# Kernel optimization log

Hardware: AMD Instinct MI355X
Metric: run time of the kernel (lower is better)

Reference implementation:

```python
import jax, jax.numpy as jnp
import numpy as np

FEATURE_DIM = 256
LN_EPS = 1e-5        # torch nn.LayerNorm default
WHITEN_EPS = 1e-4    # whitening_eps init arg


def setup_inputs() -> dict:
    key = jax.random.key(0)
    k1, _ = jax.random.split(key)
    B, T, D = 64, 2048, FEATURE_DIM
    x = jax.random.normal(k1, (B, T, D), dtype=jnp.float32)
    gamma = jnp.ones((D,), dtype=jnp.float32)
    beta = jnp.zeros((D,), dtype=jnp.float32)
    return {"x": x, "gamma": gamma, "beta": beta}


def reference(x, gamma, beta):
    # x: (B, T, D)
    B, T, D = x.shape
    # LayerNorm over last dim
    mean = jnp.mean(x, axis=-1, keepdims=True)
    var = jnp.mean((x - mean) ** 2, axis=-1, keepdims=True)
    xn = (x - mean) * jax.lax.rsqrt(var + LN_EPS) * gamma + beta
    # Batched cross-frame covariance whitening (T >= 2 here)
    mu = jnp.mean(xn, axis=1, keepdims=True)          # (B, 1, D)
    xc = xn - mu                                       # (B, T, D)
    cov = jnp.einsum('btd,bte->bde', xc, xc) / (T - 1) # (B, D, D)
    cov = cov + WHITEN_EPS * jnp.eye(D, dtype=x.dtype)
    eigvals, eigvecs = jnp.linalg.eigh(cov)            # (B, D), (B, D, D)
    inv_sqrt_vals = jax.lax.rsqrt(jnp.clip(eigvals, WHITEN_EPS, None))  # (B, D)
    # inv_sqrt = V diag(w^-1/2) V^T
    inv_sqrt = jnp.einsum('bde,be,bfe->bdf', eigvecs, inv_sqrt_vals, eigvecs)
    out = jnp.einsum('btd,bdf->btf', xc, inv_sqrt)
    return out
```

## Files before the change

kernel.cpp:

```cpp
#include <hip/hip_runtime.h>
#include <cstddef>

#define TT 2048
#define BB 64
#define DD 256
#define LN_EPS 1e-5f
#define WEPS 1e-4f

typedef __attribute__((ext_vector_type(8))) short short8;
typedef __attribute__((ext_vector_type(4))) float f32x4;
typedef __attribute__((ext_vector_type(8))) _Float16 f16x8;
typedef __attribute__((ext_vector_type(4))) _Float16 f16x4;

__device__ __forceinline__ unsigned short f2h(float f) {
  _Float16 h = (_Float16)f;
  return *(unsigned short*)&h;
}
__device__ __forceinline__ float h2f(unsigned short u) {
  _Float16 h = *(_Float16*)&u;
  return (float)h;
}
__device__ __forceinline__ void gload16(unsigned short* lds, const unsigned short* g) {
  __builtin_amdgcn_global_load_lds(
      (const __attribute__((address_space(1))) void*)g,
      (__attribute__((address_space(3))) void*)lds, 16, 0, 0);
}

__global__ __launch_bounds__(256) void prepass_kernel(const float* __restrict__ x,
    float* __restrict__ stats, float* __restrict__ part) {
  int c = blockIdx.x;
  int b = blockIdx.y;
  int tid = threadIdx.x;
  int wave = tid >> 6, lane = tid & 63;
  int rowbase = b * TT + c * 128 + wave * 32;
  const float* xb = x + (size_t)rowbase * DD + lane * 4;
  float a0 = 0.f, a1 = 0.f, a2 = 0.f, a3 = 0.f;
  for (int i = 0; i < 32; ++i) {
    float4 v = *(const float4*)&xb[(size_t)i * DD];
    float s  = v.x + v.y + v.z + v.w;
    float sq = v.x*v.x + v.y*v.y + v.z*v.z + v.w*v.w;
    #pragma unroll
    for (int off = 32; off; off >>= 1) { s += __shfl_xor(s, off); sq += __shfl_xor(sq, off); }
    float mean = s * (1.f/DD);
    float var  = fmaxf(sq * (1.f/DD) - mean*mean, 0.f);
    float rstd = rsqrtf(var + LN_EPS);
    if (lane == 0) {
      stats[2*(rowbase+i)]   = mean;
      stats[2*(rowbase+i)+1] = rstd;
    }
    a0 += (v.x - mean) * rstd;
    a1 += (v.y - mean) * rstd;
    a2 += (v.z - mean) * rstd;
    a3 += (v.w - mean) * rstd;
  }
  int pidx = c * 4 + wave;
  *(float4*)&part[((size_t)pidx*BB + b)*DD + lane*4] = make_float4(a0, a1, a2, a3);
}

__global__ __launch_bounds__(256) void mu_finalize_kernel(const float* __restrict__ part,
                                                          const float* __restrict__ gamma,
                                                          const float* __restrict__ beta,
                                                          float* __restrict__ mu) {
  int b = blockIdx.x;
  int d = threadIdx.x;
  float s = 0.f;
  #pragma unroll 8
  for (int c = 0; c < 64; ++c) s += part[((size_t)c*BB + b)*DD + d];
  mu[b*DD + d] = gamma[d] * s * (1.f/TT) + beta[d];
}

__global__ __launch_bounds__(256) void cov_mfma(const float* __restrict__ x,
    const float* __restrict__ stats, const float* __restrict__ gamma,
    const float* __restrict__ beta, const float* __restrict__ mu,
    unsigned short* __restrict__ Ch) {
  int flat = blockIdx.y * gridDim.x + blockIdx.x;
  int kx = flat & 7, j = flat >> 3;
  int b = (kx << 3) + j / 10;
  int tile = j - (j / 10) * 10;
  int p = 0, t = tile;
  while (t >= 4 - p) { t -= (4 - p); ++p; }
  int q = p + t;
  int i0 = p * 64, j0 = q * 64;
  bool diag = (p == q);

  __shared__ unsigned short sm[8448];
  unsigned short* sA = sm;
  unsigned short* sB = sm + 4096;
  __shared__ float sGi[64], sBi[64], sGj[64], sBj[64];

  int tid = threadIdx.x;
  const float* mub = mu + (size_t)b*DD;
  if (tid < 64) {
    sGi[tid] = gamma[i0+tid]; sBi[tid] = beta[i0+tid] - mub[i0+tid];
    sGj[tid] = gamma[j0+tid]; sBj[tid] = beta[j0+tid] - mub[j0+tid];
  }
  __syncthreads();

  int wave = tid >> 6, lane = tid & 63;
  int lr = lane & 15, lg = lane >> 4;
  int tg4 = tid >> 4;
  int dg  = tid & 15;
  int d0 = dg * 4;
  const float* xb  = x + (size_t)b*TT*DD;
  const float* stb = stats + (size_t)b*TT*2;

  float4 gi4 = *(const float4*)&sGi[d0];
  float4 bi4 = *(const float4*)&sBi[d0];
  float4 gj4 = *(const float4*)&sGj[d0];
  float4 bj4 = *(const float4*)&sBj[d0];

  int ch16 = tg4 >> 1, half = tg4 & 1;
  int widx[4];
  #pragma unroll
  for (int jj = 0; jj < 4; ++jj) {
    int dl = d0 + jj;
    int swz = (ch16 ^ (dl & 7) ^ ((dl >> 3) & 7)) & 7;
    widx[jj] = dl*64 + swz*8 + half*4;
  }

  f32x4 acc[4] = {};

  for (int k0 = 0; k0 < TT; k0 += 64) {
    int trow = k0 + tg4 * 4;
    float4 s01 = *(const float4*)&stb[2*trow];
    float4 s23 = *(const float4*)&stb[2*trow + 4];
    float mm[4] = {s01.x, s01.z, s23.x, s23.z};
    float rr[4] = {s01.y, s01.w, s23.y, s23.w};
    {
      _Float16 va[4][4];
      #pragma unroll
      for (int i = 0; i < 4; ++i) {
        float4 v = *(const float4*)&xb[(size_t)(trow+i)*DD + i0 + d0];
        va[i][0] = (_Float16)(((v.x - mm[i]) * rr[i]) * gi4.x + bi4.x);
        va[i][1] = (_Float16)(((v.y - mm[i]) * rr[i]) * gi4.y + bi4.y);
        va[i][2] = (_Float16)(((v.z - mm[i]) * rr[i]) * gi4.z + bi4.z);
        va[i][3] = (_Float16)(((v.w - mm[i]) * rr[i]) * gi4.w + bi4.w);
      }
      #pragma unroll
      for (int jj = 0; jj < 4; ++jj) {
        f16x4 w = {va[0][jj], va[1][jj], va[2][jj], va[3][jj]};
        *(f16x4*)&sA[widx[jj]] = w;
      }
    }
    if (!diag) {
      _Float16 vb[4][4];
      #pragma unroll
      for (int i = 0; i < 4; ++i) {
        float4 v = *(const float4*)&xb[(size_t)(trow+i)*DD + j0 + d0];
        vb[i][0] = (_Float16)(((v.x - mm[i]) * rr[i]) * gj4.x + bj4.x);
        vb[i][1] = (_Float16)(((v.y - mm[i]) * rr[i]) * gj4.y + bj4.y);
        vb[i][2] = (_Float16)(((v.z - mm[i]) * rr[i]) * gj4.z + bj4.z);
        vb[i][3] = (_Float16)(((v.w - mm[i]) * rr[i]) * gj4.w + bj4.w);
      }
      #pragma unroll
      for (int jj = 0; jj < 4; ++jj) {
        f16x4 w = {vb[0][jj], vb[1][jj], vb[2][jj], vb[3][jj]};
        *(f16x4*)&sB[widx[jj]] = w;
      }
    }
    __syncthreads();
    const unsigned short* pB = diag ? sA : sB;
    #pragma unroll
    for (int ks = 0; ks < 2; ++ks) {
      int rowA = wave*16 + lr;
      int cc = ks*4 + lg;
      int aoff = rowA*64 + (((cc ^ (rowA&7) ^ ((rowA>>3)&7)) & 7) << 3);
      f16x8 av = *(const f16x8*)&sA[aoff];
      #pragma unroll
      for (int n = 0; n < 4; ++n) {
        int rowB = n*16 + lr;
        int boff = rowB*64 + (((cc ^ (rowB&7) ^ ((rowB>>3)&7)) & 7) << 3);
        f16x8 bv = *(const f16x8*)&pB[boff];
        acc[n] = __builtin_amdgcn_mfma_f32_16x16x32_f16(av, bv, acc[n], 0, 0, 0);
      }
    }
    __syncthreads();
  }

  float* sC = (float*)sm;
  #pragma unroll
  for (int n = 0; n < 4; ++n)
    #pragma unroll
    for (int r = 0; r < 4; ++r)
      sC[(wave*16 + lg*4 + r)*65 + n*16 + lr] = acc[n][r];
  __syncthreads();
  unsigned short* Chb = Ch + (size_t)b*DD*DD;
  const float invTm1 = 1.f / (float)(TT - 1);
  int row = tid >> 2, cb = (tid & 3) * 16;
  int gi = i0 + row;
  unsigned short hv[16];
  #pragma unroll
  for (int e = 0; e < 16; ++e) {
    float v = sC[row*65 + cb + e] * invTm1;
    int gj = j0 + cb + e;
    if (gi == gj) v += WEPS;
    hv[e] = f2h(v);
    if (!diag) Chb[(size_t)gj*DD + gi] = hv[e];
  }
  size_t go = (size_t)gi*DD + j0 + cb;
  *(short8*)&Chb[go]     = *(short8*)&hv[0];
  *(short8*)&Chb[go + 8] = *(short8*)&hv[8];
}

__global__ __launch_bounds__(256) void power_kernel(
    const unsigned short* __restrict__ Ch, float* __restrict__ sbuf) {
  int b = blockIdx.x, tid = threadIdx.x;
  __shared__ unsigned short sC[DD*DD];
  __shared__ float v[DD];
  __shared__ float red[4];
  const unsigned short* Cb = Ch + (size_t)b*DD*DD;
  #pragma unroll
  for (int i = 0; i < 32; ++i) {
    int chunkid = i*256 + tid;
    int r = chunkid >> 5, ch = chunkid & 31;
    short8 qv = *(const short8*)&Cb[(size_t)chunkid*8];
    *(short8*)&sC[r*256 + ((ch ^ (r & 7)) << 3)] = qv;
  }
  unsigned u = (unsigned)tid * 2654435761u;
  v[tid] = 0.5f + (float)((u >> 9) & 1023) * (1.f/1024.f);
  __syncthreads();
  float lam = 1.f;
  for (int it = 0; it < 10; ++it) {
    float w = 0.f;
    #pragma unroll
    for (int ch = 0; ch < 32; ++ch) {
      short8 hq = *(const short8*)&sC[tid*256 + ((ch ^ (tid & 7)) << 3)];
      const float* vp = &v[ch*8];
      #pragma unroll
      for (int e = 0; e < 8; ++e) w += h2f((unsigned short)hq[e]) * vp[e];
    }
    float ssq = w * w;
    #pragma unroll
    for (int off = 32; off; off >>= 1) ssq += __shfl_xor(ssq, off);
    if ((tid & 63) == 0) red[tid >> 6] = ssq;
    __syncthreads();
    float nrm = sqrtf(red[0] + red[1] + red[2] + red[3]);
    lam = nrm;
    v[tid] = w / nrm;
    __syncthreads();
  }
  if (tid == 0) sbuf[b] = lam * 1.05f;
}

__device__ __forceinline__ void bgemm_tile2(
    const unsigned short* __restrict__ A, const unsigned short* __restrict__ B,
    unsigned short* __restrict__ C,
    float alpha, float diagBeta, int tilex, int b, unsigned short* sm) {
  unsigned short* sA = sm;
  unsigned short* sB = sm + 8192;

  const int tid = threadIdx.x;
  const int i0g = (tilex >> 1) * 128, j0g = (tilex & 1) * 128;
  const size_t mb = (size_t)b * DD * DD;
  const int wave = tid >> 6, lane = tid & 63;
  const int wr = wave >> 2, wc = wave & 3;
  const int lr = lane & 15, lg = lane >> 4;

  f32x4 acc[8] = {};

  for (int k0 = 0; k0 < DD; k0 += 64) {
    #pragma unroll
    for (int p2 = 0; p2 < 2; ++p2) {
      int slot = tid + p2 * 512;
      int row = slot >> 3, c = slot & 7;
      int srcc = (c ^ (row & 7)) << 3;
      size_t ga = mb + (size_t)(i0g + row) * DD + k0 + srcc;
      size_t gb = mb + (size_t)(j0g + row) * DD + k0 + srcc;
      int base = (wave * 64 + p2 * 512) * 8;
      gload16(&sA[base], A + ga);
      gload16(&sB[base], B + gb);
    }
    __syncthreads();
    #pragma unroll
    for (int ks = 0; ks < 2; ++ks) {
      int cc = ks * 4 + lg;
      f16x8 bv[2];
      #pragma unroll
      for (int n = 0; n < 2; ++n) {
        int rowB = wc * 32 + n * 16 + lr;
        int boff = rowB * 64 + ((cc ^ (rowB & 7)) * 8);
        bv[n] = *(const f16x8*)&sB[boff];
      }
      #pragma unroll
      for (int m = 0; m < 4; ++m) {
        int rowA = wr * 64 + m * 16 + lr;
        int aoff = rowA * 64 + ((cc ^ (rowA & 7)) * 8);
        f16x8 av = *(const f16x8*)&sA[aoff];
        #pragma unroll
        for (int n = 0; n < 2; ++n)
          acc[m*2+n] = __builtin_amdgcn_mfma_f32_16x16x32_f16(av, bv[n], acc[m*2+n], 0, 0, 0);
      }
    }
    __syncthreads();
  }

  #pragma unroll
  for (int m = 0; m < 4; ++m) {
    #pragma unroll
    for (int n = 0; n < 2; ++n) {
      int col = j0g + wc * 32 + n * 16 + lr;
      int row0 = i0g + wr * 64 + m * 16 + lg * 4;
      #pragma unroll
      for (int r = 0; r < 4; ++r) {
        float vv = alpha * acc[m*2+n][r];
        int row = row0 + r;
        if (row == col) vv += diagBeta;
        C[mb + (size_t)row * DD + col] = f2h(vv);
      }
    }
  }
}

__global__ __launch_bounds__(512) void bgemm_mfma2(
    const unsigned short* __restrict__ A, const unsigned short* __restrict__ B,
    unsigned short* __restrict__ C, float alpha, float diagBeta) {
  __shared__ unsigned short sm[16384];
  int flat = blockIdx.y * gridDim.x + blockIdx.x;
  int kx = flat & 7, j = flat >> 3;
  int b = (kx << 3) + (j >> 2);
  int tile = j & 3;
  bgemm_tile2(A, B, C, alpha, diagBeta, tile, b, sm);
}

__global__ __launch_bounds__(512) void bgemm_dual2(
    const unsigned short* __restrict__ A0, const unsigned short* __restrict__ B0,
    unsigned short* __restrict__ C0,
    const unsigned short* __restrict__ A1, const unsigned short* __restrict__ B1,
    unsigned short* __restrict__ C1) {
  __shared__ unsigned short sm[16384];
  int flat = blockIdx.y * gridDim.x + blockIdx.x;
  int kx = flat & 7, j = flat >> 3;
  int b = (kx << 3) + (j >> 3);
  int t8 = j & 7;
  int half = t8 >> 2, tile = t8 & 3;
  if (half == 0)
    bgemm_tile2(A0, B0, C0, 0.5f, 0.f, tile, b, sm);
  else
    bgemm_tile2(A1, B1, C1, 0.5f, 0.f, tile, b, sm);
}

__global__ __launch_bounds__(512) void bgemm_p0(
    const unsigned short* __restrict__ C, unsigned short* __restrict__ Y1,
    unsigned short* __restrict__ Z1, const float* __restrict__ sbuf) {
  __shared__ unsigned short sm[16384];
  unsigned short* sA = sm;
  unsigned short* sB = sm + 8192;
  int flat = blockIdx.y * gridDim.x + blockIdx.x;
  int kx = flat & 7, j = flat >> 3;
  int b = (kx << 3) + (j >> 2);
  int tilex = j & 3;

  const int tid = threadIdx.x;
  const int i0g = (tilex >> 1) * 128, j0g = (tilex & 1) * 128;
  const size_t mb = (size_t)b * DD * DD;
  const int wave = tid >> 6, lane = tid & 63;
  const int wr = wave >> 2, wc = wave & 3;
  const int lr = lane & 15, lg = lane >> 4;

  f32x4 acc[8] = {};

  for (int k0 = 0; k0 < DD; k0 += 64) {
    #pragma unroll
    for (int p2 = 0; p2 < 2; ++p2) {
      int slot = tid + p2 * 512;
      int row = slot >> 3, c = slot & 7;
      int srcc = (c ^ (row & 7)) << 3;
      size_t ga = mb + (size_t)(i0g + row) * DD + k0 + srcc;
      size_t gb = mb + (size_t)(j0g + row) * DD + k0 + srcc;
      int base = (wave * 64 + p2 * 512) * 8;
      gload16(&sA[base], C + ga);
      gload16(&sB[base], C + gb);
    }
    __syncthreads();
    #pragma unroll
    for (int ks = 0; ks < 2; ++ks) {
      int cc = ks * 4 + lg;
      f16x8 bv[2];
      #pragma unroll
      for (int n = 0; n < 2; ++n) {
        int rowB = wc * 32 + n * 16 + lr;
        int boff = rowB * 64 + ((cc ^ (rowB & 7)) * 8);
        bv[n] = *(const f16x8*)&sB[boff];
      }
      #pragma unroll
      for (int m = 0; m < 4; ++m) {
        int rowA = wr * 64 + m * 16 + lr;
        int aoff = rowA * 64 + ((cc ^ (rowA & 7)) * 8);
        f16x8 av = *(const f16x8*)&sA[aoff];
        #pragma unroll
        for (int n = 0; n < 2; ++n)
          acc[m*2+n] = __builtin_amdgcn_mfma_f32_16x16x32_f16(av, bv[n], acc[m*2+n], 0, 0, 0);
      }
    }
    __syncthreads();
  }

  float invs = 1.f / sbuf[b];
  float a2 = -0.5f * invs * invs;
  float a1c = 1.5f * invs;
  float z1c = -0.5f * invs;
  #pragma unroll
  for (int m = 0; m < 4; ++m) {
    #pragma unroll
    for (int n = 0; n < 2; ++n) {
      int col = j0g + wc * 32 + n * 16 + lr;
      int row0 = i0g + wr * 64 + m * 16 + lg * 4;
      #pragma unroll
      for (int r = 0; r < 4; ++r) {
        int row = row0 + r;
        float cv = h2f(C[mb + (size_t)row * DD + col]);
        float yv = a2 * acc[m*2+n][r] + a1c * cv;
        float zv = z1c * cv + ((row == col) ? 1.5f : 0.f);
        Y1[mb + (size_t)row * DD + col] = f2h(yv);
        Z1[mb + (size_t)row * DD + col] = f2h(zv);
      }
    }
  }
}

__global__ __launch_bounds__(512) void out_mfma2(const float* __restrict__ x,
    const float* __restrict__ stats, const float* __restrict__ gamma,
    const float* __restrict__ beta, const float* __restrict__ mu,
    const unsigned short* __restrict__ Z, const float* __restrict__ sbuf,
    float* __restrict__ out) {
  int flat = blockIdx.y * gridDim.x + blockIdx.x;
  int kx = flat & 7, j = flat >> 3;
  int b = (kx << 3) + (j >> 5);
  int tile = j & 31;
  int t0 = (tile >> 1) * 128, f0 = (tile & 1) * 128;
  __shared__ unsigned short sm[16384];
  unsigned short* sA = sm;
  unsigned short* sB = sm + 8192;
  __shared__ float sG[256], sBs[256];

  int tid = threadIdx.x;
  if (tid < 256) {
    sG[tid] = gamma[tid];
    sBs[tid] = beta[tid] - mu[(size_t)b*DD + tid];
  }
  __syncthreads();

  const int wave = tid >> 6, lane = tid & 63;
  const int wr = wave >> 2, wc = wave & 3;
  const int lr = lane & 15, lg = lane >> 4;
  const float* xb  = x + (size_t)b*TT*DD;
  const float* stb = stats + (size_t)b*TT*2;
  const unsigned short* Zb = Z + (size_t)b*DD*DD;

  f32x4 acc[8] = {};

  for (int k0 = 0; k0 < DD; k0 += 64) {
    #pragma unroll
    for (int p2 = 0; p2 < 2; ++p2) {
      int slot = tid + p2 * 512;
      int row = slot >> 3, c0 = slot & 7;
      int srcc = (c0 ^ (row & 7)) << 3;
      size_t gz = (size_t)(f0 + row) * DD + k0 + srcc;
      int base = (wave * 64 + p2 * 512) * 8;
      gload16(&sB[base], Zb + gz);
      int trow = t0 + row;
      float mean = stb[2*trow], rstd = stb[2*trow+1];
      const float* xr = xb + (size_t)trow*DD + k0 + c0*8;
      _Float16 h8[8];
      #pragma unroll
      for (int qq = 0; qq < 2; ++qq) {
        float4 v = *(const float4*)&xr[qq*4];
        float vvv[4] = {v.x, v.y, v.z, v.w};
        #pragma unroll
        for (int e2 = 0; e2 < 4; ++e2) {
          int d = k0 + c0*8 + qq*4 + e2;
          h8[qq*4+e2] = (_Float16)((vvv[e2] - mean) * rstd * sG[d] + sBs[d]);
        }
      }
      int ld = row * 64 + ((c0 ^ (row & 7)) * 8);
      *(f16x8*)&sA[ld] = *(f16x8*)&h8[0];
    }
    __syncthreads();
    #pragma unroll
    for (int ks = 0; ks < 2; ++ks) {
      int cc = ks * 4 + lg;
      f16x8 bv[2];
      #pragma unroll
      for (int n = 0; n < 2; ++n) {
        int rowB = wc * 32 + n * 16 + lr;
        int boff = rowB * 64 + ((cc ^ (rowB & 7)) * 8);
        bv[n] = *(const f16x8*)&sB[boff];
      }
      #pragma unroll
      for (int m = 0; m < 4; ++m) {
        int rowA = wr * 64 + m * 16 + lr;
        int aoff = rowA * 64 + ((cc ^ (rowA & 7)) * 8);
        f16x8 av = *(const f16x8*)&sA[aoff];
        #pragma unroll
        for (int n = 0; n < 2; ++n)
          acc[m*2+n] = __builtin_amdgcn_mfma_f32_16x16x32_f16(av, bv[n], acc[m*2+n], 0, 0, 0);
      }
    }
    __syncthreads();
  }

  float rs = rsqrtf(sbuf[b]);
  float* ob = out + (size_t)b*TT*DD;
  #pragma unroll
  for (int m = 0; m < 4; ++m) {
    #pragma unroll
    for (int n = 0; n < 2; ++n) {
      int col = f0 + wc * 32 + n * 16 + lr;
      int row0 = t0 + wr * 64 + m * 16 + lg * 4;
      #pragma unroll
      for (int r = 0; r < 4; ++r)
        ob[(size_t)(row0 + r)*DD + col] = acc[m*2+n][r] * rs;
    }
  }
}

extern "C" void kernel_launch(void* const* d_in, const int* in_sizes, int n_in,
                              void* d_out, int out_size, void* d_ws, size_t ws_size,
                              hipStream_t stream) {
  const float* x     = (const float*)d_in[0];
  const float* gamma = (const float*)d_in[1];
  const float* beta  = (const float*)d_in[2];
  float* out = (float*)d_out;

  float* wsf   = (float*)d_ws;
  float* stats = wsf;
  float* mu    = wsf + 262144;
  float* sbuf  = wsf + 278528;
  unsigned short* nsb = (unsigned short*)(wsf + 278784);
  const size_t MATU = (size_t)BB * DD * DD;
  unsigned short* H[5];
  for (int k = 0; k < 5; ++k) H[k] = nsb + (size_t)k * MATU;
  float* part = (float*)H[1];

  prepass_kernel<<<dim3(16, BB), 256, 0, stream>>>(x, stats, part);
  mu_finalize_kernel<<<BB, 256, 0, stream>>>(part, gamma, beta, mu);
  cov_mfma<<<dim3(10, BB), 256, 0, stream>>>(x, stats, gamma, beta, mu, H[0]);
  power_kernel<<<BB, 256, 0, stream>>>(H[0], sbuf);

  bgemm_p0<<<dim3(4, BB), 512, 0, stream>>>(H[0], H[3], H[1], sbuf);
  bgemm_mfma2<<<dim3(4, BB), 512, 0, stream>>>(H[1], H[3], H[2], -1.f, 3.f);
  bgemm_dual2<<<dim3(8, BB), 512, 0, stream>>>(H[3], H[2], H[0], H[2], H[1], H[4]);
  bgemm_mfma2<<<dim3(4, BB), 512, 0, stream>>>(H[4], H[0], H[2], -1.f, 3.f);
  bgemm_dual2<<<dim3(8, BB), 512, 0, stream>>>(H[0], H[2], H[3], H[2], H[4], H[1]);
  bgemm_mfma2<<<dim3(4, BB), 512, 0, stream>>>(H[1], H[3], H[2], -1.f, 3.f);
  bgemm_mfma2<<<dim3(4, BB), 512, 0, stream>>>(H[2], H[1], H[4], 0.5f, 0.f);

  out_mfma2<<<dim3(32, BB), 512, 0, stream>>>(x, stats, gamma, beta, mu, H[4], sbuf, out);
}
```

Before: 218.5 us.

## Double-buffer LDS stages in covariance, GEMM and output MFMA kernels

Adds ping-pong shared-memory buffers to the covariance, batched GEMM, polynomial-iteration and output kernels. The next K-slice is loaded and staged while MFMAs run on the current one, with a single barrier per iteration instead of two. The goal is to hide global-load latency behind compute. In exchange, LDS per block doubles (64 KB for the 512-thread kernels), which can reduce occupancy, and staging values held in registers add register pressure.

```diff
diff --git a/kernel.cpp b/kernel.cpp
--- a/kernel.cpp
+++ b/kernel.cpp
@@ -83,9 +83,7 @@
   int i0 = p * 64, j0 = q * 64;
   bool diag = (p == q);
 
-  __shared__ unsigned short sm[8448];
-  unsigned short* sA = sm;
-  unsigned short* sB = sm + 4096;
+  __shared__ unsigned short sm[16384];
   __shared__ float sGi[64], sBi[64], sGj[64], sBj[64];
 
   int tid = threadIdx.x;
@@ -120,52 +118,64 @@
 
   f32x4 acc[4] = {};
 
-  for (int k0 = 0; k0 < TT; k0 += 64) {
-    int trow = k0 + tg4 * 4;
-    float4 s01 = *(const float4*)&stb[2*trow];
-    float4 s23 = *(const float4*)&stb[2*trow + 4];
-    float mm[4] = {s01.x, s01.z, s23.x, s23.z};
-    float rr[4] = {s01.y, s01.w, s23.y, s23.w};
-    {
-      _Float16 va[4][4];
-      #pragma unroll
-      for (int i = 0; i < 4; ++i) {
-        float4 v = *(const float4*)&xb[(size_t)(trow+i)*DD + i0 + d0];
-        va[i][0] = (_Float16)(((v.x - mm[i]) * rr[i]) * gi4.x + bi4.x);
-        va[i][1] = (_Float16)(((v.y - mm[i]) * rr[i]) * gi4.y + bi4.y);
-        va[i][2] = (_Float16)(((v.z - mm[i]) * rr[i]) * gi4.z + bi4.z);
-        va[i][3] = (_Float16)(((v.w - mm[i]) * rr[i]) * gi4.w + bi4.w);
-      }
-      #pragma unroll
-      for (int jj = 0; jj < 4; ++jj) {
-        f16x4 w = {va[0][jj], va[1][jj], va[2][jj], va[3][jj]};
-        *(f16x4*)&sA[widx[jj]] = w;
-      }
-    }
-    if (!diag) {
-      _Float16 vb[4][4];
-      #pragma unroll
-      for (int i = 0; i < 4; ++i) {
-        float4 v = *(const float4*)&xb[(size_t)(trow+i)*DD + j0 + d0];
-        vb[i][0] = (_Float16)(((v.x - mm[i]) * rr[i]) * gj4.x + bj4.x);
-        vb[i][1] = (_Float16)(((v.y - mm[i]) * rr[i]) * gj4.y + bj4.y);
-        vb[i][2] = (_Float16)(((v.z - mm[i]) * rr[i]) * gj4.z + bj4.z);
-        vb[i][3] = (_Float16)(((v.w - mm[i]) * rr[i]) * gj4.w + bj4.w);
-      }
-      #pragma unroll
-      for (int jj = 0; jj < 4; ++jj) {
-        f16x4 w = {vb[0][jj], vb[1][jj], vb[2][jj], vb[3][jj]};
-        *(f16x4*)&sB[widx[jj]] = w;
-      }
-    }
-    __syncthreads();
-    const unsigned short* pB = diag ? sA : sB;
+  #define COV_STAGE(k0v, dst)                                                  \
+  {                                                                            \
+    int trow = (k0v) + tg4 * 4;                                                \
+    float4 s01 = *(const float4*)&stb[2*trow];                                 \
+    float4 s23 = *(const float4*)&stb[2*trow + 4];                             \
+    float mm[4] = {s01.x, s01.z, s23.x, s23.z};                                \
+    float rr[4] = {s01.y, s01.w, s23.y, s23.w};                                \
+    {                                                                          \
+      _Float16 va[4][4];                                                       \
+      _Pragma("unroll")                                                        \
+      for (int i = 0; i < 4; ++i) {                                            \
+        float4 v = *(const float4*)&xb[(size_t)(trow+i)*DD + i0 + d0];         \
+        va[i][0] = (_Float16)(((v.x - mm[i]) * rr[i]) * gi4.x + bi4.x);        \
+        va[i][1] = (_Float16)(((v.y - mm[i]) * rr[i]) * gi4.y + bi4.y);        \
+        va[i][2] = (_Float16)(((v.z - mm[i]) * rr[i]) * gi4.z + bi4.z);        \
+        va[i][3] = (_Float16)(((v.w - mm[i]) * rr[i]) * gi4.w + bi4.w);        \
+      }                                                                        \
+      _Pragma("unroll")                                                        \
+      for (int jj = 0; jj < 4; ++jj) {                                         \
+        f16x4 w = {va[0][jj], va[1][jj], va[2][jj], va[3][jj]};                \
+        *(f16x4*)&(dst)[widx[jj]] = w;                                         \
+      }                                                                        \
+    }                                                                          \
+    if (!diag) {                                                               \
+      _Float16 vb[4][4];                                                       \
+      _Pragma("unroll")                                                        \
+      for (int i = 0; i < 4; ++i) {                                            \
+        float4 v = *(const float4*)&xb[(size_t)(trow+i)*DD + j0 + d0];         \
+        vb[i][0] = (_Float16)(((v.x - mm[i]) * rr[i]) * gj4.x + bj4.x);        \
+        vb[i][1] = (_Float16)(((v.y - mm[i]) * rr[i]) * gj4.y + bj4.y);        \
+        vb[i][2] = (_Float16)(((v.z - mm[i]) * rr[i]) * gj4.z + bj4.z);        \
+        vb[i][3] = (_Float16)(((v.w - mm[i]) * rr[i]) * gj4.w + bj4.w);        \
+      }                                                                        \
+      _Pragma("unroll")                                                        \
+      for (int jj = 0; jj < 4; ++jj) {                                         \
+        f16x4 w = {vb[0][jj], vb[1][jj], vb[2][jj], vb[3][jj]};                \
+        *(f16x4*)&(dst)[4096 + widx[jj]] = w;                                  \
+      }                                                                        \
+    }                                                                          \
+  }
+
+  COV_STAGE(0, sm);
+  __syncthreads();
+
+  for (int kk = 0; kk < 32; ++kk) {
+    unsigned short* cur = sm + (kk & 1) * 8192;
+    if (kk < 31) {
+      unsigned short* nxt = sm + ((kk & 1) ^ 1) * 8192;
+      COV_STAGE((kk + 1) * 64, nxt);
+    }
+    const unsigned short* pA = cur;
+    const unsigned short* pB = diag ? cur : (cur + 4096);
     #pragma unroll
     for (int ks = 0; ks < 2; ++ks) {
       int rowA = wave*16 + lr;
       int cc = ks*4 + lg;
       int aoff = rowA*64 + (((cc ^ (rowA&7) ^ ((rowA>>3)&7)) & 7) << 3);
-      f16x8 av = *(const f16x8*)&sA[aoff];
+      f16x8 av = *(const f16x8*)&pA[aoff];
       #pragma unroll
       for (int n = 0; n < 4; ++n) {
         int rowB = n*16 + lr;
@@ -176,6 +186,7 @@
     }
     __syncthreads();
   }
+  #undef COV_STAGE
 
   float* sC = (float*)sm;
   #pragma unroll
@@ -246,9 +257,6 @@
     const unsigned short* __restrict__ A, const unsigned short* __restrict__ B,
     unsigned short* __restrict__ C,
     float alpha, float diagBeta, int tilex, int b, unsigned short* sm) {
-  unsigned short* sA = sm;
-  unsigned short* sB = sm + 8192;
-
   const int tid = threadIdx.x;
   const int i0g = (tilex >> 1) * 128, j0g = (tilex & 1) * 128;
   const size_t mb = (size_t)b * DD * DD;
@@ -258,19 +266,33 @@
 
   f32x4 acc[8] = {};
 
-  for (int k0 = 0; k0 < DD; k0 += 64) {
-    #pragma unroll
-    for (int p2 = 0; p2 < 2; ++p2) {
-      int slot = tid + p2 * 512;
-      int row = slot >> 3, c = slot & 7;
-      int srcc = (c ^ (row & 7)) << 3;
-      size_t ga = mb + (size_t)(i0g + row) * DD + k0 + srcc;
-      size_t gb = mb + (size_t)(j0g + row) * DD + k0 + srcc;
-      int base = (wave * 64 + p2 * 512) * 8;
-      gload16(&sA[base], A + ga);
-      gload16(&sB[base], B + gb);
-    }
-    __syncthreads();
+  #pragma unroll
+  for (int p2 = 0; p2 < 2; ++p2) {
+    int slot = tid + p2 * 512;
+    int row = slot >> 3, c = slot & 7;
+    int srcc = (c ^ (row & 7)) << 3;
+    int base = (wave * 64 + p2 * 512) * 8;
+    gload16(&sm[base], A + mb + (size_t)(i0g + row) * DD + srcc);
+    gload16(&sm[8192 + base], B + mb + (size_t)(j0g + row) * DD + srcc);
+  }
+  __syncthreads();
+
+  #pragma unroll
+  for (int kk = 0; kk < 4; ++kk) {
+    unsigned short* cur = sm + (kk & 1) * 16384;
+    if (kk < 3) {
+      unsigned short* nxt = sm + ((kk & 1) ^ 1) * 16384;
+      int k0n = (kk + 1) * 64;
+      #pragma unroll
+      for (int p2 = 0; p2 < 2; ++p2) {
+        int slot = tid + p2 * 512;
+        int row = slot >> 3, c = slot & 7;
+        int srcc = (c ^ (row & 7)) << 3;
+        int base = (wave * 64 + p2 * 512) * 8;
+        gload16(&nxt[base], A + mb + (size_t)(i0g + row) * DD + k0n + srcc);
+        gload16(&nxt[8192 + base], B + mb + (size_t)(j0g + row) * DD + k0n + srcc);
+      }
+    }
     #pragma unroll
     for (int ks = 0; ks < 2; ++ks) {
       int cc = ks * 4 + lg;
@@ -279,13 +301,13 @@
       for (int n = 0; n < 2; ++n) {
         int rowB = wc * 32 + n * 16 + lr;
         int boff = rowB * 64 + ((cc ^ (rowB & 7)) * 8);
-        bv[n] = *(const f16x8*)&sB[boff];
+        bv[n] = *(const f16x8*)&cur[8192 + boff];
       }
       #pragma unroll
       for (int m = 0; m < 4; ++m) {
         int rowA = wr * 64 + m * 16 + lr;
         int aoff = rowA * 64 + ((cc ^ (rowA & 7)) * 8);
-        f16x8 av = *(const f16x8*)&sA[aoff];
+        f16x8 av = *(const f16x8*)&cur[aoff];
         #pragma unroll
         for (int n = 0; n < 2; ++n)
           acc[m*2+n] = __builtin_amdgcn_mfma_f32_16x16x32_f16(av, bv[n], acc[m*2+n], 0, 0, 0);
@@ -314,7 +336,7 @@
 __global__ __launch_bounds__(512) void bgemm_mfma2(
     const unsigned short* __restrict__ A, const unsigned short* __restrict__ B,
     unsigned short* __restrict__ C, float alpha, float diagBeta) {
-  __shared__ unsigned short sm[16384];
+  __shared__ unsigned short sm[32768];
   int flat = blockIdx.y * gridDim.x + blockIdx.x;
   int kx = flat & 7, j = flat >> 3;
   int b = (kx << 3) + (j >> 2);
@@ -327,7 +349,7 @@
     unsigned short* __restrict__ C0,
     const unsigned short* __restrict__ A1, const unsigned short* __restrict__ B1,
     unsigned short* __restrict__ C1) {
-  __shared__ unsigned short sm[16384];
+  __shared__ unsigned short sm[32768];
   int flat = blockIdx.y * gridDim.x + blockIdx.x;
   int kx = flat & 7, j = flat >> 3;
   int b = (kx << 3) + (j >> 3);
@@ -342,9 +364,7 @@
 __global__ __launch_bounds__(512) void bgemm_p0(
     const unsigned short* __restrict__ C, unsigned short* __restrict__ Y1,
     unsigned short* __restrict__ Z1, const float* __restrict__ sbuf) {
-  __shared__ unsigned short sm[16384];
-  unsigned short* sA = sm;
-  unsigned short* sB = sm + 8192;
+  __shared__ unsigned short sm[32768];
   int flat = blockIdx.y * gridDim.x + blockIdx.x;
   int kx = flat & 7, j = flat >> 3;
   int b = (kx << 3) + (j >> 2);
@@ -359,19 +379,33 @@
 
   f32x4 acc[8] = {};
 
-  for (int k0 = 0; k0 < DD; k0 += 64) {
-    #pragma unroll
-    for (int p2 = 0; p2 < 2; ++p2) {
-      int slot = tid + p2 * 512;
-      int row = slot >> 3, c = slot & 7;
-      int srcc = (c ^ (row & 7)) << 3;
-      size_t ga = mb + (size_t)(i0g + row) * DD + k0 + srcc;
-      size_t gb = mb + (size_t)(j0g + row) * DD + k0 + srcc;
-      int base = (wave * 64 + p2 * 512) * 8;
-      gload16(&sA[base], C + ga);
-      gload16(&sB[base], C + gb);
-    }
-    __syncthreads();
+  #pragma unroll
+  for (int p2 = 0; p2 < 2; ++p2) {
+    int slot = tid + p2 * 512;
+    int row = slot >> 3, c = slot & 7;
+    int srcc = (c ^ (row & 7)) << 3;
+    int base = (wave * 64 + p2 * 512) * 8;
+    gload16(&sm[base], C + mb + (size_t)(i0g + row) * DD + srcc);
+    gload16(&sm[8192 + base], C + mb + (size_t)(j0g + row) * DD + srcc);
+  }
+  __syncthreads();
+
+  #pragma unroll
+  for (int kk = 0; kk < 4; ++kk) {
+    unsigned short* cur = sm + (kk & 1) * 16384;
+    if (kk < 3) {
+      unsigned short* nxt = sm + ((kk & 1) ^ 1) * 16384;
+      int k0n = (kk + 1) * 64;
+      #pragma unroll
+      for (int p2 = 0; p2 < 2; ++p2) {
+        int slot = tid + p2 * 512;
+        int row = slot >> 3, c = slot & 7;
+        int srcc = (c ^ (row & 7)) << 3;
+        int base = (wave * 64 + p2 * 512) * 8;
+        gload16(&nxt[base], C + mb + (size_t)(i0g + row) * DD + k0n + srcc);
+        gload16(&nxt[8192 + base], C + mb + (size_t)(j0g + row) * DD + k0n + srcc);
+      }
+    }
     #pragma unroll
     for (int ks = 0; ks < 2; ++ks) {
       int cc = ks * 4 + lg;
@@ -380,13 +414,13 @@
       for (int n = 0; n < 2; ++n) {
         int rowB = wc * 32 + n * 16 + lr;
         int boff = rowB * 64 + ((cc ^ (rowB & 7)) * 8);
-        bv[n] = *(const f16x8*)&sB[boff];
+        bv[n] = *(const f16x8*)&cur[8192 + boff];
       }
       #pragma unroll
       for (int m = 0; m < 4; ++m) {
         int rowA = wr * 64 + m * 16 + lr;
         int aoff = rowA * 64 + ((cc ^ (rowA & 7)) * 8);
-        f16x8 av = *(const f16x8*)&sA[aoff];
+        f16x8 av = *(const f16x8*)&cur[aoff];
         #pragma unroll
         for (int n = 0; n < 2; ++n)
           acc[m*2+n] = __builtin_amdgcn_mfma_f32_16x16x32_f16(av, bv[n], acc[m*2+n], 0, 0, 0);
@@ -428,9 +462,7 @@
   int b = (kx << 3) + (j >> 5);
   int tile = j & 31;
   int t0 = (tile >> 1) * 128, f0 = (tile & 1) * 128;
-  __shared__ unsigned short sm[16384];
-  unsigned short* sA = sm;
-  unsigned short* sB = sm + 8192;
+  __shared__ unsigned short sm[32768];
   __shared__ float sG[256], sBs[256];
 
   int tid = threadIdx.x;
@@ -449,33 +481,45 @@
 
   f32x4 acc[8] = {};
 
-  for (int k0 = 0; k0 < DD; k0 += 64) {
-    #pragma unroll
-    for (int p2 = 0; p2 < 2; ++p2) {
-      int slot = tid + p2 * 512;
-      int row = slot >> 3, c0 = slot & 7;
-      int srcc = (c0 ^ (row & 7)) << 3;
-      size_t gz = (size_t)(f0 + row) * DD + k0 + srcc;
-      int base = (wave * 64 + p2 * 512) * 8;
-      gload16(&sB[base], Zb + gz);
-      int trow = t0 + row;
-      float mean = stb[2*trow], rstd = stb[2*trow+1];
-      const float* xr = xb + (size_t)trow*DD + k0 + c0*8;
-      _Float16 h8[8];
-      #pragma unroll
-      for (int qq = 0; qq < 2; ++qq) {
-        float4 v = *(const float4*)&xr[qq*4];
-        float vvv[4] = {v.x, v.y, v.z, v.w};
-        #pragma unroll
-        for (int e2 = 0; e2 < 4; ++e2) {
-          int d = k0 + c0*8 + qq*4 + e2;
-          h8[qq*4+e2] = (_Float16)((vvv[e2] - mean) * rstd * sG[d] + sBs[d]);
-        }
-      }
-      int ld = row * 64 + ((c0 ^ (row & 7)) * 8);
-      *(f16x8*)&sA[ld] = *(f16x8*)&h8[0];
-    }
-    __syncthreads();
+  #define OUT_STAGE(k0v, dst)                                                  \
+  {                                                                            \
+    _Pragma("unroll")                                                          \
+    for (int p2 = 0; p2 < 2; ++p2) {                                           \
+      int slot = tid + p2 * 512;                                               \
+      int row = slot >> 3, c0 = slot & 7;                                      \
+      int srcc = (c0 ^ (row & 7)) << 3;                                        \
+      size_t gz = (size_t)(f0 + row) * DD + (k0v) + srcc;                      \
+      int base = (wave * 64 + p2 * 512) * 8;                                   \
+      gload16(&(dst)[8192 + base], Zb + gz);                                   \
+      int trow = t0 + row;                                                     \
+      float mean = stb[2*trow], rstd = stb[2*trow+1];                          \
+      const float* xr = xb + (size_t)trow*DD + (k0v) + c0*8;                   \
+      _Float16 h8[8];                                                          \
+      _Pragma("unroll")                                                        \
+      for (int qq = 0; qq < 2; ++qq) {                                         \
+        float4 v = *(const float4*)&xr[qq*4];                                  \
+        float vvv[4] = {v.x, v.y, v.z, v.w};                                   \
+        _Pragma("unroll")                                                      \
+        for (int e2 = 0; e2 < 4; ++e2) {                                       \
+          int d = (k0v) + c0*8 + qq*4 + e2;                                    \
+          h8[qq*4+e2] = (_Float16)((vvv[e2] - mean) * rstd * sG[d] + sBs[d]);  \
+        }                                                                      \
+      }                                                                        \
+      int ld = row * 64 + ((c0 ^ (row & 7)) * 8);                              \
+      *(f16x8*)&(dst)[ld] = *(f16x8*)&h8[0];                                   \
+    }                                                                          \
+  }
+
+  OUT_STAGE(0, sm);
+  __syncthreads();
+
+  #pragma unroll
+  for (int kk = 0; kk < 4; ++kk) {
+    unsigned short* cur = sm + (kk & 1) * 16384;
+    if (kk < 3) {
+      unsigned short* nxt = sm + ((kk & 1) ^ 1) * 16384;
+      OUT_STAGE((kk + 1) * 64, nxt);
+    }
     #pragma unroll
     for (int ks = 0; ks < 2; ++ks) {
       int cc = ks * 4 + lg;
@@ -484,13 +528,13 @@
       for (int n = 0; n < 2; ++n) {
         int rowB = wc * 32 + n * 16 + lr;
         int boff = rowB * 64 + ((cc ^ (rowB & 7)) * 8);
-        bv[n] = *(const f16x8*)&sB[boff];
+        bv[n] = *(const f16x8*)&cur[8192 + boff];
       }
       #pragma unroll
       for (int m = 0; m < 4; ++m) {
         int rowA = wr * 64 + m * 16 + lr;
         int aoff = rowA * 64 + ((cc ^ (rowA & 7)) * 8);
-        f16x8 av = *(const f16x8*)&sA[aoff];
+        f16x8 av = *(const f16x8*)&cur[aoff];
         #pragma unroll
         for (int n = 0; n < 2; ++n)
           acc[m*2+n] = __builtin_amdgcn_mfma_f32_16x16x32_f16(av, bv[n], acc[m*2+n], 0, 0, 0);
@@ -498,6 +542,7 @@
     }
     __syncthreads();
   }
+  #undef OUT_STAGE
 
   float rs = rsqrtf(sbuf[b]);
   float* ob = out + (size_t)b*TT*DD;
```

Result: no change. 220.2 us (+0.8%).
